# Performance work log

Measured on AMD Instinct MI355X. Metric: run time of the kernel, lower is better.

The kernel has to match this reference:

```python
import jax, jax.numpy as jnp
import numpy as np

T, B, D, H = 512, 64, 512, 512


def setup_inputs() -> dict:
    key = jax.random.key(0)
    ks = jax.random.split(key, 7)
    stdv = 1.0 / np.sqrt(H)
    u = lambda k, shape: jax.random.uniform(k, shape, jnp.float32, -stdv, stdv)
    return {
        'x': jax.random.normal(ks[0], (T, B, D), jnp.float32),
        'h0': jax.random.normal(ks[1], (B, H), jnp.float32),
        'c0': jax.random.normal(ks[2], (B, H), jnp.float32),
        'w_ih': u(ks[3], (4 * H, D)),
        'b_ih': u(ks[4], (4 * H,)),
        'w_hh': u(ks[5], (4 * H, H)),
        'b_hh': u(ks[6], (4 * H,)),
    }


def reference(x, h0, c0, w_ih, b_ih, w_hh, b_hh):
    # One LSTM layer, forward direction, no dropout, no PackedSequence.
    # gates = Linear_ih(x_t) + Linear_hh(h_{t-1}); split into i,f,g,o along features.
    def step(carry, x_t):
        h, c = carry
        gates = x_t @ w_ih.T + b_ih + h @ w_hh.T + b_hh  # [B, 4H]
        i_g, f_g, g_g, o_g = jnp.split(gates, 4, axis=1)
        c_t = jax.nn.sigmoid(f_g) * c + jax.nn.sigmoid(i_g) * jnp.tanh(g_g)
        h_t = jax.nn.sigmoid(o_g) * jnp.tanh(c_t)
        return (h_t, c_t), h_t

    (h_last, c_last), h_all = jax.lax.scan(step, (h0, c0), x)
    # output [T, B, H], final states [B, H]
    return h_all, h_last, c_last
```

## Files before the change

### kernel.cpp

```cpp
#include <hip/hip_runtime.h>
#include <stdint.h>

#define T_STEPS 512
#define BATCH   64
#define DIM     512
#define NGROUP  4
#define WG_PER_GROUP 32
#define GB      16
#define TBH     (T_STEPS*BATCH*DIM)
#define BH      (BATCH*DIM)
#define TAGM    0x00010001u

typedef __attribute__((ext_vector_type(8))) short short8;
typedef __attribute__((ext_vector_type(4))) float f32x4;
typedef __attribute__((ext_vector_type(4))) unsigned int u32x4;
typedef unsigned short u16;

__device__ __forceinline__ u16 f2bf(float f) {
  union { float f; uint32_t u; } c; c.f = f;
  uint32_t u = c.u;
  return (u16)((u + 0x7FFFu + ((u >> 16) & 1u)) >> 16);
}

__device__ __forceinline__ float fsigmoid(float x) {
  float e = __expf(-x);
  return __builtin_amdgcn_rcpf(1.f + e);
}
__device__ __forceinline__ float ftanh(float x) {
  float e = __expf(2.f * x);
  return 1.f - 2.f * __builtin_amdgcn_rcpf(e + 1.f);
}

__global__ void pack_w_kernel(const float* __restrict__ w_ih,
                              const float* __restrict__ w_hh,
                              uint4* __restrict__ wpack) {
  int j = blockIdx.x;
  for (int u = threadIdx.x; u < 8192; u += 256) {
    int w    = u >> 11;
    int kt   = (u >> 6) & 31;
    int lane = u & 63;
    int n  = w * 512 + j * 16 + (lane & 15);
    int k0 = kt * 32 + 8 * (lane >> 4);
    const float* src = (k0 < 512) ? (w_ih + (size_t)n * 512 + k0)
                                  : (w_hh + (size_t)n * 512 + (k0 - 512));
    uint32_t p0 = f2bf(src[0]) | ((uint32_t)f2bf(src[1]) << 16);
    uint32_t p1 = f2bf(src[2]) | ((uint32_t)f2bf(src[3]) << 16);
    uint32_t p2 = f2bf(src[4]) | ((uint32_t)f2bf(src[5]) << 16);
    uint32_t p3 = f2bf(src[6]) | ((uint32_t)f2bf(src[7]) << 16);
    wpack[(size_t)j * 8192 + u] = make_uint4(p0, p1, p2, p3);
  }
}

__global__ void pack_x_kernel(const float* __restrict__ x, uint4* __restrict__ xbf) {
  size_t i = (size_t)blockIdx.x * 256 + threadIdx.x;
  const float4* src = (const float4*)x + i * 2;
  float4 a = src[0], b = src[1];
  uint32_t p0 = f2bf(a.x) | ((uint32_t)f2bf(a.y) << 16);
  uint32_t p1 = f2bf(a.z) | ((uint32_t)f2bf(a.w) << 16);
  uint32_t p2 = f2bf(b.x) | ((uint32_t)f2bf(b.y) << 16);
  uint32_t p3 = f2bf(b.z) | ((uint32_t)f2bf(b.w) << 16);
  xbf[i] = make_uint4(p0, p1, p2, p3);
}

__launch_bounds__(256, 1)
__global__ void lstm_persist(const float* __restrict__ h0, const float* __restrict__ c0,
                             const float* __restrict__ b_ih, const float* __restrict__ b_hh,
                             const uint4* __restrict__ wpack, const u16* __restrict__ xbf,
                             u16* __restrict__ h_buf, float* __restrict__ out) {
  __shared__ uint4 w_lds[8192];
  __shared__ float c_lds[4][16][16];

  const int tid  = threadIdx.x;
  const int lane = tid & 63;
  const int wv   = tid >> 6;
  const int wg   = blockIdx.x;
  const int grp  = wg >> 5;
  const int wgj  = wg & 31;
  const int B0   = grp * GB;

  for (int i = tid; i < 8192; i += 256) w_lds[i] = wpack[(size_t)wgj * 8192 + i];

  const int pb   = tid >> 4;
  const int pc   = tid & 15;
  const int colg = wgj * 16 + pc;
  float c_reg = c0[(B0 + pb) * DIM + colg];
  const float bias0 = b_ih[0*512 + colg] + b_hh[0*512 + colg];
  const float bias1 = b_ih[1*512 + colg] + b_hh[1*512 + colg];
  const float bias2 = b_ih[2*512 + colg] + b_hh[2*512 + colg];
  const float bias3 = b_ih[3*512 + colg] + b_hh[3*512 + colg];

  const int m  = lane & 15;
  const int kq = 8 * (lane >> 4);

  const short8* wl = (const short8*)w_lds;

  __syncthreads();

  {
    float h0f = h0[(B0 + pb) * DIM + colg];
    float h0n = __shfl_xor(h0f, 1);
    if (!(pc & 1)) {
      uint32_t both = (uint32_t)f2bf(h0f) | ((uint32_t)f2bf(h0n) << 16);
      uint32_t v = (both & ~TAGM) | TAGM;
      uint32_t* p = (uint32_t*)(h_buf + ((size_t)(0 * NGROUP + grp) * GB + pb) * DIM + colg);
      __hip_atomic_store(p, v, __ATOMIC_RELAXED, __HIP_MEMORY_SCOPE_AGENT);
    }
  }

  f32x4 xacc;
  {
    f32x4 a0 = (f32x4){0.f,0.f,0.f,0.f}, a1 = (f32x4){0.f,0.f,0.f,0.f};
    const u16* xrow = xbf + (size_t)(0 * BATCH + B0 + m) * DIM;
    for (int kt = 0; kt < 16; kt += 2) {
      short8 a = *((const short8*)(xrow + kt * 32 + kq));
      a0 = __builtin_amdgcn_mfma_f32_16x16x32_bf16(a, wl[(wv*32+kt)*64+lane], a0, 0,0,0);
      short8 a2 = *((const short8*)(xrow + (kt+1) * 32 + kq));
      a1 = __builtin_amdgcn_mfma_f32_16x16x32_bf16(a2, wl[(wv*32+kt+1)*64+lane], a1, 0,0,0);
    }
    xacc = a0 + a1;
  }

  for (int t = 0; t < T_STEPS; ++t) {
    const int pr = t & 1;
    const u16* tb = h_buf + (size_t)(pr * NGROUP + grp) * GB * DIM;
    const uint32_t e = 1u ^ (((uint32_t)t >> 1) & 1u);

    union HU { u32x4 u; short8 s; } hq[16];
    {
      uint64_t pa2 = (uint64_t)tb + (uint64_t)(m * 1024 + (lane >> 4) * 16);
      int spins = 0;
      for (;;) {
#define HLOAD(i, lit)                                                          \
        asm volatile("global_load_dwordx4 %0, %1, off offset:" lit " sc0 sc1"  \
                     : "=v"(hq[i].u) : "v"(pa2) : "memory");
        HLOAD(0,"0")    HLOAD(1,"64")   HLOAD(2,"128")  HLOAD(3,"192")
        HLOAD(4,"256")  HLOAD(5,"320")  HLOAD(6,"384")  HLOAD(7,"448")
        HLOAD(8,"512")  HLOAD(9,"576")  HLOAD(10,"640") HLOAD(11,"704")
        HLOAD(12,"768") HLOAD(13,"832") HLOAD(14,"896") HLOAD(15,"960")
#undef HLOAD
        asm volatile("s_waitcnt vmcnt(0)" ::: "memory");
        __builtin_amdgcn_sched_barrier(0);
        uint32_t andv = 0xFFFFFFFFu, orv = 0u;
        #pragma unroll
        for (int i = 0; i < 16; ++i) {
          u32x4 v = hq[i].u;
          andv &= v.x & v.y & v.z & v.w;
          orv  |= v.x | v.y | v.z | v.w;
        }
        uint32_t ok = e ? ((andv & TAGM) == TAGM) : ((orv & TAGM) == 0u);
        if (__ballot(ok != 0u) == ~0ull) break;
        if (++spins > (1 << 16)) break;
      }
      __builtin_amdgcn_sched_barrier(0);
    }

    f32x4 acc0 = xacc, acc1 = (f32x4){0.f,0.f,0.f,0.f};
    #pragma unroll
    for (int kt = 0; kt < 16; kt += 2) {
      acc0 = __builtin_amdgcn_mfma_f32_16x16x32_bf16(hq[kt].s,   wl[(wv*32+16+kt)*64+lane],   acc0, 0,0,0);
      acc1 = __builtin_amdgcn_mfma_f32_16x16x32_bf16(hq[kt+1].s, wl[(wv*32+16+kt+1)*64+lane], acc1, 0,0,0);
    }
    f32x4 acc = acc0 + acc1;

    {
      int r0 = (lane >> 4) * 4;
      c_lds[wv][r0 + 0][lane & 15] = acc[0];
      c_lds[wv][r0 + 1][lane & 15] = acc[1];
      c_lds[wv][r0 + 2][lane & 15] = acc[2];
      c_lds[wv][r0 + 3][lane & 15] = acc[3];
    }
    __syncthreads();

    float gi = fsigmoid(c_lds[0][pb][pc] + bias0);
    float gf = fsigmoid(c_lds[1][pb][pc] + bias1);
    float gg = ftanh  (c_lds[2][pb][pc] + bias2);
    float go = fsigmoid(c_lds[3][pb][pc] + bias3);
    c_reg = gf * c_reg + gi * gg;
    float h = go * ftanh(c_reg);

    if (t < T_STEPS - 1) {
      {
        float hn = __shfl_xor(h, 1);
        if (!(pc & 1)) {
          uint32_t both = (uint32_t)f2bf(h) | ((uint32_t)f2bf(hn) << 16);
          const uint32_t tagw = 1u ^ ((((uint32_t)t + 1) >> 1) & 1u);
          uint32_t v = (both & ~TAGM) | (tagw * TAGM);
          uint32_t* p = (uint32_t*)(h_buf + ((size_t)((pr ^ 1) * NGROUP + grp) * GB + pb) * DIM + colg);
          __hip_atomic_store(p, v, __ATOMIC_RELAXED, __HIP_MEMORY_SCOPE_AGENT);
        }
      }
      out[((size_t)t * BATCH + B0 + pb) * DIM + colg] = h;
      f32x4 a2_0 = (f32x4){0.f,0.f,0.f,0.f}, a2_1 = (f32x4){0.f,0.f,0.f,0.f};
      const u16* xr = xbf + (size_t)((t + 1) * BATCH + B0 + m) * DIM;
      for (int kt = 0; kt < 16; kt += 2) {
        short8 a = *((const short8*)(xr + kt * 32 + kq));
        a2_0 = __builtin_amdgcn_mfma_f32_16x16x32_bf16(a, wl[(wv*32+kt)*64+lane], a2_0, 0,0,0);
        short8 a2 = *((const short8*)(xr + (kt+1) * 32 + kq));
        a2_1 = __builtin_amdgcn_mfma_f32_16x16x32_bf16(a2, wl[(wv*32+kt+1)*64+lane], a2_1, 0,0,0);
      }
      xacc = a2_0 + a2_1;
    } else {
      out[((size_t)t * BATCH + B0 + pb) * DIM + colg] = h;
      out[TBH + (B0 + pb) * DIM + colg]      = h;
      out[TBH + BH + (B0 + pb) * DIM + colg] = c_reg;
    }
  }
}

extern "C" void kernel_launch(void* const* d_in, const int* in_sizes, int n_in,
                              void* d_out, int out_size, void* d_ws, size_t ws_size,
                              hipStream_t stream) {
  (void)in_sizes; (void)n_in; (void)out_size; (void)ws_size;
  const float* x    = (const float*)d_in[0];
  const float* h0   = (const float*)d_in[1];
  const float* c0   = (const float*)d_in[2];
  const float* w_ih = (const float*)d_in[3];
  const float* b_ih = (const float*)d_in[4];
  const float* w_hh = (const float*)d_in[5];
  const float* b_hh = (const float*)d_in[6];
  float* out = (float*)d_out;

  char* ws = (char*)d_ws;
  uint4* wpack = (uint4*)ws;
  u16*   xbf   = (u16*)(ws + ((size_t)4 << 20));
  u16*   hbuf  = (u16*)(ws + ((size_t)36 << 20));

  pack_w_kernel<<<dim3(32),   dim3(256), 0, stream>>>(w_ih, w_hh, wpack);
  pack_x_kernel<<<dim3(8192), dim3(256), 0, stream>>>(x, (uint4*)xbf);

  void* args[] = {(void*)&h0, (void*)&c0, (void*)&b_ih, (void*)&b_hh,
                  (void*)&wpack, (void*)&xbf, (void*)&hbuf, (void*)&out};
  hipError_t e = hipLaunchCooperativeKernel((void*)lstm_persist, dim3(NGROUP * WG_PER_GROUP),
                                            dim3(256), args, 0, stream);
  if (e != hipSuccess) {
    lstm_persist<<<dim3(NGROUP * WG_PER_GROUP), dim3(256), 0, stream>>>(
        h0, c0, b_ih, b_hh, wpack, xbf, hbuf, out);
  }
}
```

Baseline: 2.657 ms.

## Split batch into eight groups and poll h-buffer with adaptive cache flags

Raises the batch groups from four to eight with eight rows each, interleaving workgroup-to-group mapping so 256 workgroups share the recurrence and each MFMA tile duplicates its 8 rows into the 16-row slot. The polling loop first issues loads with only sc0 and switches to sc0 sc1 coherent loads after a spin threshold, aiming to cut polling cost while keeping eventual visibility. In exchange it wastes half of each MFMA on duplicated rows, and the sc0-only loads may return stale data until the threshold is reached. The launch grid is assumed to have been enlarged in the unseen host code.

```diff
diff --git a/kernel.cpp b/kernel.cpp
--- a/kernel.cpp
+++ b/kernel.cpp
@@ -4,9 +4,9 @@
 #define T_STEPS 512
 #define BATCH   64
 #define DIM     512
-#define NGROUP  4
+#define NGROUP  8
 #define WG_PER_GROUP 32
-#define GB      16
+#define GB      8
 #define TBH     (T_STEPS*BATCH*DIM)
 #define BH      (BATCH*DIM)
 #define TAGM    0x00010001u
@@ -74,8 +74,8 @@
   const int lane = tid & 63;
   const int wv   = tid >> 6;
   const int wg   = blockIdx.x;
-  const int grp  = wg >> 5;
-  const int wgj  = wg & 31;
+  const int grp  = wg & 7;
+  const int wgj  = wg >> 3;
   const int B0   = grp * GB;
 
   for (int i = tid; i < 8192; i += 256) w_lds[i] = wpack[(size_t)wgj * 8192 + i];
@@ -83,23 +83,26 @@
   const int pb   = tid >> 4;
   const int pc   = tid & 15;
   const int colg = wgj * 16 + pc;
-  float c_reg = c0[(B0 + pb) * DIM + colg];
+  const int pbs  = pb & 7;
+  float c_reg = c0[(B0 + pbs) * DIM + colg];
   const float bias0 = b_ih[0*512 + colg] + b_hh[0*512 + colg];
   const float bias1 = b_ih[1*512 + colg] + b_hh[1*512 + colg];
   const float bias2 = b_ih[2*512 + colg] + b_hh[2*512 + colg];
   const float bias3 = b_ih[3*512 + colg] + b_hh[3*512 + colg];
 
   const int m  = lane & 15;
+  const int m8 = lane & 7;
   const int kq = 8 * (lane >> 4);
 
   const short8* wl = (const short8*)w_lds;
+  bool sticky = false;
 
   __syncthreads();
 
   {
-    float h0f = h0[(B0 + pb) * DIM + colg];
+    float h0f = h0[(B0 + pbs) * DIM + colg];
     float h0n = __shfl_xor(h0f, 1);
-    if (!(pc & 1)) {
+    if (pb < GB && !(pc & 1)) {
       uint32_t both = (uint32_t)f2bf(h0f) | ((uint32_t)f2bf(h0n) << 16);
       uint32_t v = (both & ~TAGM) | TAGM;
       uint32_t* p = (uint32_t*)(h_buf + ((size_t)(0 * NGROUP + grp) * GB + pb) * DIM + colg);
@@ -110,7 +113,7 @@
   f32x4 xacc;
   {
     f32x4 a0 = (f32x4){0.f,0.f,0.f,0.f}, a1 = (f32x4){0.f,0.f,0.f,0.f};
-    const u16* xrow = xbf + (size_t)(0 * BATCH + B0 + m) * DIM;
+    const u16* xrow = xbf + (size_t)(0 * BATCH + B0 + m8) * DIM;
     for (int kt = 0; kt < 16; kt += 2) {
       short8 a = *((const short8*)(xrow + kt * 32 + kq));
       a0 = __builtin_amdgcn_mfma_f32_16x16x32_bf16(a, wl[(wv*32+kt)*64+lane], a0, 0,0,0);
@@ -124,20 +127,35 @@
     const int pr = t & 1;
     const u16* tb = h_buf + (size_t)(pr * NGROUP + grp) * GB * DIM;
     const uint32_t e = 1u ^ (((uint32_t)t >> 1) & 1u);
+    const int esc = (t < 2) ? 256 : 48;
 
     union HU { u32x4 u; short8 s; } hq[16];
     {
-      uint64_t pa2 = (uint64_t)tb + (uint64_t)(m * 1024 + (lane >> 4) * 16);
+      uint64_t pa2 = (uint64_t)tb + (uint64_t)(m8 * 1024 + (lane >> 4) * 16);
       int spins = 0;
       for (;;) {
-#define HLOAD(i, lit)                                                          \
-        asm volatile("global_load_dwordx4 %0, %1, off offset:" lit " sc0 sc1"  \
-                     : "=v"(hq[i].u) : "v"(pa2) : "memory");
-        HLOAD(0,"0")    HLOAD(1,"64")   HLOAD(2,"128")  HLOAD(3,"192")
-        HLOAD(4,"256")  HLOAD(5,"320")  HLOAD(6,"384")  HLOAD(7,"448")
-        HLOAD(8,"512")  HLOAD(9,"576")  HLOAD(10,"640") HLOAD(11,"704")
-        HLOAD(12,"768") HLOAD(13,"832") HLOAD(14,"896") HLOAD(15,"960")
-#undef HLOAD
+#define HLOADS(FLAGS)                                                          \
+  do {                                                                         \
+    asm volatile("global_load_dwordx4 %0, %1, off offset:0 "   FLAGS : "=v"(hq[0].u)  : "v"(pa2) : "memory"); \
+    asm volatile("global_load_dwordx4 %0, %1, off offset:64 "  FLAGS : "=v"(hq[1].u)  : "v"(pa2) : "memory"); \
+    asm volatile("global_load_dwordx4 %0, %1, off offset:128 " FLAGS : "=v"(hq[2].u)  : "v"(pa2) : "memory"); \
+    asm volatile("global_load_dwordx4 %0, %1, off offset:192 " FLAGS : "=v"(hq[3].u)  : "v"(pa2) : "memory"); \
+    asm volatile("global_load_dwordx4 %0, %1, off offset:256 " FLAGS : "=v"(hq[4].u)  : "v"(pa2) : "memory"); \
+    asm volatile("global_load_dwordx4 %0, %1, off offset:320 " FLAGS : "=v"(hq[5].u)  : "v"(pa2) : "memory"); \
+    asm volatile("global_load_dwordx4 %0, %1, off offset:384 " FLAGS : "=v"(hq[6].u)  : "v"(pa2) : "memory"); \
+    asm volatile("global_load_dwordx4 %0, %1, off offset:448 " FLAGS : "=v"(hq[7].u)  : "v"(pa2) : "memory"); \
+    asm volatile("global_load_dwordx4 %0, %1, off offset:512 " FLAGS : "=v"(hq[8].u)  : "v"(pa2) : "memory"); \
+    asm volatile("global_load_dwordx4 %0, %1, off offset:576 " FLAGS : "=v"(hq[9].u)  : "v"(pa2) : "memory"); \
+    asm volatile("global_load_dwordx4 %0, %1, off offset:640 " FLAGS : "=v"(hq[10].u) : "v"(pa2) : "memory"); \
+    asm volatile("global_load_dwordx4 %0, %1, off offset:704 " FLAGS : "=v"(hq[11].u) : "v"(pa2) : "memory"); \
+    asm volatile("global_load_dwordx4 %0, %1, off offset:768 " FLAGS : "=v"(hq[12].u) : "v"(pa2) : "memory"); \
+    asm volatile("global_load_dwordx4 %0, %1, off offset:832 " FLAGS : "=v"(hq[13].u) : "v"(pa2) : "memory"); \
+    asm volatile("global_load_dwordx4 %0, %1, off offset:896 " FLAGS : "=v"(hq[14].u) : "v"(pa2) : "memory"); \
+    asm volatile("global_load_dwordx4 %0, %1, off offset:960 " FLAGS : "=v"(hq[15].u) : "v"(pa2) : "memory"); \
+  } while (0)
+        if (!sticky) HLOADS("sc0");
+        else         HLOADS("sc0 sc1");
+#undef HLOADS
         asm volatile("s_waitcnt vmcnt(0)" ::: "memory");
         __builtin_amdgcn_sched_barrier(0);
         uint32_t andv = 0xFFFFFFFFu, orv = 0u;
@@ -149,7 +167,8 @@
         }
         uint32_t ok = e ? ((andv & TAGM) == TAGM) : ((orv & TAGM) == 0u);
         if (__ballot(ok != 0u) == ~0ull) break;
-        if (++spins > (1 << 16)) break;
+        if (++spins == esc) sticky = true;
+        if (spins > (1 << 16)) break;
       }
       __builtin_amdgcn_sched_barrier(0);
     }
@@ -171,17 +190,17 @@
     }
     __syncthreads();
 
-    float gi = fsigmoid(c_lds[0][pb][pc] + bias0);
-    float gf = fsigmoid(c_lds[1][pb][pc] + bias1);
-    float gg = ftanh  (c_lds[2][pb][pc] + bias2);
-    float go = fsigmoid(c_lds[3][pb][pc] + bias3);
+    float gi = fsigmoid(c_lds[0][pbs][pc] + bias0);
+    float gf = fsigmoid(c_lds[1][pbs][pc] + bias1);
+    float gg = ftanh  (c_lds[2][pbs][pc] + bias2);
+    float go = fsigmoid(c_lds[3][pbs][pc] + bias3);
     c_reg = gf * c_reg + gi * gg;
     float h = go * ftanh(c_reg);
 
     if (t < T_STEPS - 1) {
       {
         float hn = __shfl_xor(h, 1);
-        if (!(pc & 1)) {
+        if (pb < GB && !(pc & 1)) {
           uint32_t both = (uint32_t)f2bf(h) | ((uint32_t)f2bf(hn) << 16);
           const uint32_t tagw = 1u ^ ((((uint32_t)t + 1) >> 1) & 1u);
           uint32_t v = (both & ~TAGM) | (tagw * TAGM);
@@ -189,9 +208,9 @@
           __hip_atomic_store(p, v, __ATOMIC_RELAXED, __HIP_MEMORY_SCOPE_AGENT);
         }
       }
-      out[((size_t)t * BATCH + B0 + pb) * DIM + colg] = h;
+      if (pb < GB) out[((size_t)t * BATCH + B0 + pb) * DIM + colg] = h;
       f32x4 a2_0 = (f32x4){0.f,0.f,0.f,0.f}, a2_1 = (f32x4){0.f,0.f,0.f,0.f};
-      const u16* xr = xbf + (size_t)((t + 1) * BATCH + B0 + m) * DIM;
+      const u16* xr = xbf + (size_t)((t + 1) * BATCH + B0 + m8) * DIM;
       for (int kt = 0; kt < 16; kt += 2) {
         short8 a = *((const short8*)(xr + kt * 32 + kq));
         a2_0 = __builtin_amdgcn_mfma_f32_16x16x32_bf16(a, wl[(wv*32+kt)*64+lane], a2_0, 0,0,0);
@@ -199,7 +218,7 @@
         a2_1 = __builtin_amdgcn_mfma_f32_16x16x32_bf16(a2, wl[(wv*32+kt+1)*64+lane], a2_1, 0,0,0);
       }
       xacc = a2_0 + a2_1;
-    } else {
+    } else if (pb < GB) {
       out[((size_t)t * BATCH + B0 + pb) * DIM + colg] = h;
       out[TBH + (B0 + pb) * DIM + colg]      = h;
       out[TBH + BH + (B0 + pb) * DIM + colg] = c_reg;
```

Result: slower. 2.897 ms (+9.0%).
